# Optimization experiments

Hardware: AMD Instinct MI355X
Metric: run time of the kernel (lower is better)

Reference implementation:

```python
import jax, jax.numpy as jnp
import numpy as np

B, LQ, LA, D, H = 8, 2048, 2048, 300, 150

def setup_inputs() -> dict:
    key = jax.random.key(0)
    ks = jax.random.split(key, 6)
    return {
        "Q": jax.random.normal(ks[0], (B, LQ, D), dtype=jnp.float32),
        "A": jax.random.normal(ks[1], (B, LA, D), dtype=jnp.float32),
        "Wi": jax.random.normal(ks[2], (D, H), dtype=jnp.float32) * (1.0 / np.sqrt(D)),
        "Wu": jax.random.normal(ks[3], (D, H), dtype=jnp.float32) * (1.0 / np.sqrt(D)),
        "Wg": jax.random.normal(ks[4], (H, H), dtype=jnp.float32) * (1.0 / np.sqrt(H)),
        "Wt": jax.random.normal(ks[5], (2 * H, H), dtype=jnp.float32) * (1.0 / np.sqrt(2 * H)),
        "bi": jnp.zeros((H,), dtype=jnp.float32),
        "bu": jnp.zeros((H,), dtype=jnp.float32),
        "bg": jnp.zeros((H,), dtype=jnp.float32),
        "bt": jnp.zeros((H,), dtype=jnp.float32),
    }

def reference(Q, A, Wi, Wu, Wg, Wt, bi, bu, bg, bt):
    # sigmoid/tanh gated projections (shared weights for Q and A)
    def gate(X):
        return jax.nn.sigmoid(X @ Wi + bi) * jnp.tanh(X @ Wu + bu)
    Qh = gate(Q)  # [B, LQ, H]
    Ah = gate(A)  # [B, LA, H]
    # attention scores G[b,q,a] = <(Qh Wg + bg)[b,q], Ah[b,a]>
    G = jnp.einsum('bqh,bah->bqa', Qh @ Wg + bg, Ah)
    G = jax.nn.softmax(G, axis=1)  # softmax over Q positions
    # H[b,a] = sum_q G[b,q,a] * Qh[b,q]
    Hm = jnp.einsum('bqa,bqh->bah', G, Qh)  # [B, LA, H]
    # 'nn' comparison: relu(concat([Ah, Hm]) @ Wt + bt)
    T = jax.nn.relu(jnp.concatenate([Ah, Hm], axis=-1) @ Wt + bt)
    return T
```

## Files before the change

### kernel.cpp

```cpp
#include <hip/hip_runtime.h>
#include <math.h>

#define BB 8
#define LQ 2048
#define DD 300
#define HHH 150
#define NROWS (BB * LQ)

#define KP 168
#define QTS 72
#define WCE 27136
#define SLAB_B 45056
#define SLAB_E 22528
#define QHT_OFF_E 11008

typedef __bf16 bf16x8 __attribute__((ext_vector_type(8)));
typedef __bf16 bf16x4 __attribute__((ext_vector_type(4)));
typedef float f32x16 __attribute__((ext_vector_type(16)));

__device__ __forceinline__ void gl_lds16(const void* g, void* l) {
    __builtin_amdgcn_global_load_lds(
        (const __attribute__((address_space(1))) void*)g,
        (__attribute__((address_space(3))) void*)l,
        16, 0, 0);
}
__device__ __forceinline__ void stage_flat(const void* g, void* l, int bytes,
                                           int w, int lane) {
    for (int ofs = w * 1024; ofs < bytes; ofs += 4096)
        gl_lds16((const char*)g + ofs + lane * 16, (char*)l + ofs);
}
__device__ __forceinline__ void stage_flat8(const void* g, void* l, int bytes,
                                            int w, int lane) {
    for (int ofs = w * 1024; ofs < bytes; ofs += 8192)
        gl_lds16((const char*)g + ofs + lane * 16, (char*)l + ofs);
}
__device__ __forceinline__ f32x16 z16() {
    f32x16 v;
#pragma unroll
    for (int i = 0; i < 16; i++) v[i] = 0.f;
    return v;
}
__device__ __forceinline__ bf16x8 cvt8(float4 u, float4 v) {
    return (bf16x8){(__bf16)u.x, (__bf16)u.y, (__bf16)u.z, (__bf16)u.w,
                    (__bf16)v.x, (__bf16)v.y, (__bf16)v.z, (__bf16)v.w};
}

__global__ __launch_bounds__(256) void convert_weights(
    const float* __restrict__ Wi, const float* __restrict__ Wu,
    const float* __restrict__ Wg, const float* __restrict__ Wt,
    __bf16* __restrict__ WiC, __bf16* __restrict__ WuC,
    __bf16* __restrict__ WgT, __bf16* __restrict__ Wt12)
{
    const int z = blockIdx.y;
    const int i = blockIdx.x * 256 + threadIdx.x;
    if (z < 2) {
        if (i >= 2 * WCE) return;
        int c = i / WCE, rem = i - c * WCE;
        float v = 0.f;
        if (rem < 160 * KP) {
            int h = rem / KP, kc = rem - h * KP;
            int d = c * 160 + kc;
            if (kc < 160 && d < DD && h < HHH) v = (z ? Wu : Wi)[(size_t)d * HHH + h];
        }
        (z ? WuC : WiC)[i] = (__bf16)v;
    } else if (z == 2) {
        if (i >= WCE) return;
        float v = 0.f;
        if (i < 160 * KP) {
            int h = i / KP, kc = i - h * KP;
            if (kc < HHH && h < HHH) v = Wg[(size_t)kc * HHH + h];
        }
        WgT[i] = (__bf16)v;
    } else {
        if (i >= 2 * 160 * KP) return;
        int c = i / (160 * KP), rem = i - c * (160 * KP);
        int h = rem / KP, kc = rem - h * KP;
        float v = (kc < HHH && h < HHH) ? Wt[(size_t)(c * HHH + kc) * HHH + h] : 0.f;
        Wt12[i] = (__bf16)v;
    }
}

__global__ __launch_bounds__(512, 2) void gatep(
    const float* __restrict__ Q, const float* __restrict__ A,
    const __bf16* __restrict__ WiC, const __bf16* __restrict__ WuC,
    const __bf16* __restrict__ WgT,
    const float* __restrict__ bi, const float* __restrict__ bu,
    const float* __restrict__ bg,
    __bf16* __restrict__ AhB, __bf16* __restrict__ Slab)
{
    __shared__ __align__(16) __bf16 WB[2][WCE];
    __shared__ __align__(16) __bf16 QhA[128 * KP];
    const int tid = threadIdx.x;
    const int w = tid >> 6, lane = tid & 63;
    const int m32 = lane & 31, half = lane >> 5;
    const int wm = w & 3, wn = w >> 2;
    const int tof = wn ? 3 : 0, tn = wn ? 2 : 3;
    const int z = blockIdx.y;
    const int r0 = blockIdx.x * 128;
    const float* X = z ? A : Q;

    stage_flat8(WiC, WB[0], 54272, w, lane);

    const float* xrow = X + (size_t)(r0 + wm * 32 + m32) * DD + half * 8;
    bf16x8 af0[10], af1[10];
#pragma unroll
    for (int ks = 0; ks < 10; ks++) {
        float4 u = *(const float4*)(xrow + ks * 16);
        float4 v = *(const float4*)(xrow + ks * 16 + 4);
        af0[ks] = cvt8(u, v);
    }

    f32x16 ai[3], au[3];
#pragma unroll
    for (int t = 0; t < 3; t++) { ai[t] = z16(); au[t] = z16(); }

    __syncthreads();
    stage_flat8(WuC, WB[1], 54272, w, lane);

#pragma unroll
    for (int ks = 0; ks < 8; ks++) {
        float4 u = *(const float4*)(xrow + 160 + ks * 16);
        float4 v = *(const float4*)(xrow + 160 + ks * 16 + 4);
        af1[ks] = cvt8(u, v);
    }
    {
        float4 u = *(const float4*)(xrow + 288);
        float4 v = (half == 0) ? *(const float4*)(xrow + 292) : (float4){0.f, 0.f, 0.f, 0.f};
        af1[8] = cvt8(u, v);
        af1[9] = (bf16x8){(__bf16)0.f, (__bf16)0.f, (__bf16)0.f, (__bf16)0.f,
                          (__bf16)0.f, (__bf16)0.f, (__bf16)0.f, (__bf16)0.f};
    }

    for (int ks = 0; ks < 10; ks++)
#pragma unroll
        for (int ti = 0; ti < 3; ti++)
            if (ti < tn)
                ai[ti] = __builtin_amdgcn_mfma_f32_32x32x16_bf16(
                    af0[ks], *(const bf16x8*)(WB[0] + ((tof + ti) * 32 + m32) * KP + ks * 16 + half * 8),
                    ai[ti], 0, 0, 0);
    __syncthreads();
    stage_flat8(WiC + WCE, WB[0], 54272, w, lane);
    for (int ks = 0; ks < 10; ks++)
#pragma unroll
        for (int ti = 0; ti < 3; ti++)
            if (ti < tn)
                au[ti] = __builtin_amdgcn_mfma_f32_32x32x16_bf16(
                    af0[ks], *(const bf16x8*)(WB[1] + ((tof + ti) * 32 + m32) * KP + ks * 16 + half * 8),
                    au[ti], 0, 0, 0);
    __syncthreads();
    stage_flat8(WuC + WCE, WB[1], 54272, w, lane);
    for (int ks = 0; ks < 10; ks++)
#pragma unroll
        for (int ti = 0; ti < 3; ti++)
            if (ti < tn)
                ai[ti] = __builtin_amdgcn_mfma_f32_32x32x16_bf16(
                    af1[ks], *(const bf16x8*)(WB[0] + ((tof + ti) * 32 + m32) * KP + ks * 16 + half * 8),
                    ai[ti], 0, 0, 0);
    __syncthreads();
    if (z == 0) stage_flat8(WgT, WB[0], 54272, w, lane);
    for (int ks = 0; ks < 10; ks++)
#pragma unroll
        for (int ti = 0; ti < 3; ti++)
            if (ti < tn)
                au[ti] = __builtin_amdgcn_mfma_f32_32x32x16_bf16(
                    af1[ks], *(const bf16x8*)(WB[1] + ((tof + ti) * 32 + m32) * KP + ks * 16 + half * 8),
                    au[ti], 0, 0, 0);

#pragma unroll
    for (int ti = 0; ti < 3; ti++) {
        if (ti >= tn) continue;
        int h = (tof + ti) * 32 + m32;
        int hc = h < HHH ? h : 0;
        float bih = bi[hc], buh = bu[hc];
#pragma unroll
        for (int r = 0; r < 16; r++) {
            float v = 0.f;
            if (h < HHH) {
                float xi = ai[ti][r] + bih, xu = au[ti][r] + buh;
                float s = 1.f / (1.f + __expf(-xi));
                float tt = 1.f - 2.f / (1.f + __expf(2.f * xu));
                v = s * tt;
            }
            ai[ti][r] = v;
        }
    }

    if (z) {
#pragma unroll
        for (int ti = 0; ti < 3; ti++) {
            if (ti >= tn) continue;
            int h = (tof + ti) * 32 + m32;
#pragma unroll
            for (int r = 0; r < 16; r++) {
                int rowp = (r & 3) + 8 * (r >> 2) + 4 * half;
                AhB[(size_t)(r0 + wm * 32 + rowp) * KP + h] = (__bf16)ai[ti][r];
            }
        }
        return;
    }

#pragma unroll
    for (int ti = 0; ti < 3; ti++) {
        if (ti >= tn) continue;
        int h = (tof + ti) * 32 + m32;
#pragma unroll
        for (int r = 0; r < 16; r++) {
            int rowp = (r & 3) + 8 * (r >> 2) + 4 * half;
            QhA[(wm * 32 + rowp) * KP + h] = (__bf16)ai[ti][r];
        }
    }
    __syncthreads();

    bf16x8 afq[10];
#pragma unroll
    for (int ks = 0; ks < 10; ks++)
        afq[ks] = *(const bf16x8*)(QhA + (wm * 32 + m32) * KP + ks * 16 + half * 8);

    f32x16 qg[3];
#pragma unroll
    for (int t = 0; t < 3; t++) qg[t] = z16();
    for (int ks = 0; ks < 10; ks++)
#pragma unroll
        for (int ti = 0; ti < 3; ti++)
            if (ti < tn)
                qg[ti] = __builtin_amdgcn_mfma_f32_32x32x16_bf16(
                    afq[ks], *(const bf16x8*)(WB[0] + ((tof + ti) * 32 + m32) * KP + ks * 16 + half * 8),
                    qg[ti], 0, 0, 0);

    const int b = r0 >> 11, qt0 = (r0 & 2047) >> 6;
#pragma unroll
    for (int ti = 0; ti < 3; ti++) {
        if (ti >= tn) continue;
        int h = (tof + ti) * 32 + m32;
        int hc = h < HHH ? h : 0;
        float bgh = bg[hc];
#pragma unroll
        for (int r = 0; r < 16; r++) {
            int rowp = (r & 3) + 8 * (r >> 2) + 4 * half;
            int q = (r0 & 2047) + wm * 32 + rowp;
            float v = (h < HHH) ? (qg[ti][r] + bgh) : 0.f;
            Slab[(size_t)(b * 32 + (q >> 6)) * SLAB_E + (q & 63) * KP + h] = (__bf16)v;
        }
    }

    {
        const int jl = tid & 63, tile = (tid >> 6) & 1, hgrp = tid >> 7;
        for (int hseg = hgrp; hseg < 20; hseg += 4) {
            bf16x8 vv = *(const bf16x8*)(QhA + (tile * 64 + jl) * KP + hseg * 8);
            __bf16* dst = Slab + (size_t)(b * 32 + qt0 + tile) * SLAB_E + QHT_OFF_E + jl;
#pragma unroll
            for (int e = 0; e < 8; e++)
                dst[(hseg * 8 + e) * QTS] = vv[e];
        }
    }
}

__global__ __launch_bounds__(512, 2) void attn_mfma(
    const __bf16* __restrict__ Slab, const __bf16* __restrict__ AhB,
    __bf16* __restrict__ O, float* __restrict__ L)
{
    __shared__ __align__(16) __bf16 Buf[2][SLAB_E];
    __shared__ __align__(16) __bf16 PS[128 * QTS];
    const int tid = threadIdx.x;
    const int w = tid >> 6, lane = tid & 63;
    const int m32 = lane & 31, half = lane >> 5;
    const int wa = w & 3, wx = w >> 2;
    const int b = blockIdx.y, qh = blockIdx.z;
    const int a0 = blockIdx.x * 128;

    const char* slabBase = (const char*)Slab + (size_t)(b * 32 + qh * 16) * SLAB_B;
    stage_flat8(slabBase, Buf[0], SLAB_B, w, lane);

    const __bf16* arow = AhB + (size_t)(b * LQ + a0 + wa * 32 + m32) * KP + half * 8;
    bf16x8 af[10];
#pragma unroll
    for (int ks = 0; ks < 10; ks++)
        af[ks] = *(const bf16x8*)(arow + ks * 16);

    float lsum[16];
#pragma unroll
    for (int r = 0; r < 16; r++) lsum[r] = 0.f;
    f32x16 acc[5];
#pragma unroll
    for (int t = 0; t < 5; t++) acc[t] = z16();
    __syncthreads();

    for (int qt = 0; qt < 16; qt++) {
        const int cur = qt & 1;
        if (qt < 15)
            stage_flat8(slabBase + (size_t)(qt + 1) * SLAB_B, Buf[cur ^ 1], SLAB_B, w, lane);
        const __bf16* Bq = Buf[cur];
        const __bf16* Bv = Buf[cur] + QHT_OFF_E;

        f32x16 s = z16();
        for (int ks = 0; ks < 10; ks++)
            s = __builtin_amdgcn_mfma_f32_32x32x16_bf16(
                af[ks], *(const bf16x8*)(Bq + (wx * 32 + m32) * KP + ks * 16 + half * 8),
                s, 0, 0, 0);

#pragma unroll
        for (int r = 0; r < 16; r++) {
            int rowp = (r & 3) + 8 * (r >> 2) + 4 * half;
            float p = __expf(s[r]);
            lsum[r] += p;
            PS[(wa * 32 + rowp) * QTS + wx * 32 + m32] = (__bf16)p;
        }

#pragma unroll
        for (int kkL = 0; kkL < 2; kkL++) {
            bf16x8 pf = *(const bf16x8*)(PS + (wa * 32 + m32) * QTS + (wx * 2 + kkL) * 16 + half * 8);
#pragma unroll
            for (int t = 0; t < 5; t++)
                acc[t] = __builtin_amdgcn_mfma_f32_32x32x16_bf16(
                    pf, *(const bf16x8*)(Bv + (t * 32 + m32) * QTS + (wx * 2 + kkL) * 16 + half * 8),
                    acc[t], 0, 0, 0);
        }
        __syncthreads();
    }

#pragma unroll
    for (int r = 0; r < 16; r++) {
        float s = lsum[r];
#pragma unroll
        for (int m = 1; m < 32; m <<= 1) s += __shfl_xor(s, m, 64);
        lsum[r] = s;
    }
    const int part = qh * 2 + wx;
    __bf16* Ob = O + ((size_t)part * NROWS + b * LQ + a0 + wa * 32) * 160;
#pragma unroll
    for (int t = 0; t < 5; t++) {
        int h = t * 32 + m32;
#pragma unroll
        for (int r = 0; r < 16; r++) {
            int rowp = (r & 3) + 8 * (r >> 2) + 4 * half;
            Ob[(size_t)rowp * 160 + h] = (__bf16)acc[t][r];
        }
    }
    if (m32 == 0) {
        float* Lb = L + (size_t)part * NROWS + b * LQ + a0 + wa * 32;
#pragma unroll
        for (int r = 0; r < 16; r++) {
            int rowp = (r & 3) + 8 * (r >> 2) + 4 * half;
            Lb[rowp] = lsum[r];
        }
    }
}

__global__ __launch_bounds__(256, 1) void final_mfma(
    const __bf16* __restrict__ AhB, const __bf16* __restrict__ O,
    const float* __restrict__ L, const __bf16* __restrict__ Wt12,
    const float* __restrict__ bt, float* __restrict__ Out)
{
    __shared__ __align__(16) __bf16 AS[64 * KP];
    __shared__ __align__(16) __bf16 HS[64 * KP];
    __shared__ __align__(16) __bf16 WtS[2 * 160 * KP];
    const int tid = threadIdx.x;
    const int w = tid >> 6, lane = tid & 63;
    const int m32 = lane & 31, half = lane >> 5;
    const int r0 = blockIdx.x * 64;

    stage_flat(AhB + (size_t)r0 * KP, AS, 21504, w, lane);
    stage_flat(Wt12, WtS, 107520, w, lane);

    {
        int rhat = tid >> 2, qq = tid & 3;
        int grow = r0 + rhat;
        float inv = 1.f / (L[grow] + L[NROWS + grow] + L[2 * NROWS + grow] + L[3 * NROWS + grow]);
#pragma unroll
        for (int k = 0; k < 5; k++) {
            float sum[8];
#pragma unroll
            for (int j = 0; j < 8; j++) sum[j] = 0.f;
#pragma unroll
            for (int p = 0; p < 4; p++) {
                bf16x8 x = *(const bf16x8*)(O + ((size_t)p * NROWS + grow) * 160 + qq * 40 + k * 8);
#pragma unroll
                for (int j = 0; j < 8; j++) sum[j] += (float)x[j];
            }
            bf16x8 hv;
#pragma unroll
            for (int j = 0; j < 8; j++) hv[j] = (__bf16)(sum[j] * inv);
            *(bf16x8*)(HS + rhat * KP + qq * 40 + k * 8) = hv;
        }
    }
    __syncthreads();

    const int m = w & 1, th = w >> 1;
    const int tbase = th ? 3 : 0, tn = th ? 2 : 3;
    f32x16 acc[3];
#pragma unroll
    for (int i = 0; i < 3; i++) acc[i] = z16();

    for (int ch = 0; ch < 2; ch++) {
        const __bf16* src = ch ? HS : AS;
        for (int ks = 0; ks < 10; ks++) {
            bf16x8 af = *(const bf16x8*)(src + (m * 32 + m32) * KP + ks * 16 + half * 8);
#pragma unroll
            for (int ti = 0; ti < 3; ti++) {
                if (ti < tn) {
                    int t = tbase + ti;
                    acc[ti] = __builtin_amdgcn_mfma_f32_32x32x16_bf16(
                        af, *(const bf16x8*)(WtS + (ch * 160 + t * 32 + m32) * KP + ks * 16 + half * 8),
                        acc[ti], 0, 0, 0);
                }
            }
        }
    }

#pragma unroll
    for (int ti = 0; ti < 3; ti++) {
        if (ti < tn) {
            int t = tbase + ti;
            int h = t * 32 + m32;
            if (h < HHH) {
                float bth = bt[h];
#pragma unroll
                for (int r = 0; r < 16; r++) {
                    int rowp = (r & 3) + 8 * (r >> 2) + 4 * half;
                    float v = acc[ti][r] + bth;
                    Out[(size_t)(r0 + m * 32 + rowp) * HHH + h] = v > 0.f ? v : 0.f;
                }
            }
        }
    }
}

extern "C" void kernel_launch(void* const* d_in, const int* in_sizes, int n_in,
                              void* d_out, int out_size, void* d_ws, size_t ws_size,
                              hipStream_t stream)
{
    const float* Q  = (const float*)d_in[0];
    const float* A  = (const float*)d_in[1];
    const float* Wi = (const float*)d_in[2];
    const float* Wu = (const float*)d_in[3];
    const float* Wg = (const float*)d_in[4];
    const float* Wt = (const float*)d_in[5];
    const float* bi = (const float*)d_in[6];
    const float* bu = (const float*)d_in[7];
    const float* bg = (const float*)d_in[8];
    const float* bt = (const float*)d_in[9];
    float* out = (float*)d_out;

    char* ws = (char*)d_ws;
    __bf16* Slab = (__bf16*)(ws);
    __bf16* AhB  = (__bf16*)(ws + 11534336);
    __bf16* Op   = (__bf16*)(ws + 17039360);
    float*  Lp   = (float*) (ws + 38010880);
    __bf16* WiC  = (__bf16*)(ws + 38273024);
    __bf16* WuC  = (__bf16*)(ws + 38381568);
    __bf16* WgT  = (__bf16*)(ws + 38490112);
    __bf16* Wt12 = (__bf16*)(ws + 38544384);

    convert_weights<<<dim3(212, 4), 256, 0, stream>>>(Wi, Wu, Wg, Wt,
                                                      WiC, WuC, WgT, Wt12);
    gatep<<<dim3(NROWS / 128, 2), 512, 0, stream>>>(Q, A, WiC, WuC, WgT,
                                                    bi, bu, bg, AhB, Slab);
    attn_mfma<<<dim3(16, BB, 2), 512, 0, stream>>>(Slab, AhB, Op, Lp);
    final_mfma<<<NROWS / 64, 256, 0, stream>>>(AhB, Op, Lp, Wt12, bt, out);
}
```

Baseline: 167.3 us.

## Retile attention kernel so each wave owns 32 A rows across full Q tile

The attention kernel now gives each of its 8 waves 32 distinct A rows (256 rows per block) and has each wave cover the whole 64-wide Q tile, instead of splitting the Q tile between two waves. The Q range per block halves to 8 tiles and the grid gains a fourth Q partition. This removes the duplicated A-row work across waves and halves the number of slab tiles each block streams, raising MFMA work per staged LDS tile. In exchange it adds a larger PS buffer in LDS, more accumulator registers per wave, and four partial outputs instead of four per row, so occupancy may change.

```diff
diff --git a/kernel.cpp b/kernel.cpp
--- a/kernel.cpp
+++ b/kernel.cpp
@@ -260,18 +260,17 @@
     __bf16* __restrict__ O, float* __restrict__ L)
 {
     __shared__ __align__(16) __bf16 Buf[2][SLAB_E];
-    __shared__ __align__(16) __bf16 PS[128 * QTS];
+    __shared__ __align__(16) __bf16 PS[256 * QTS];
     const int tid = threadIdx.x;
     const int w = tid >> 6, lane = tid & 63;
     const int m32 = lane & 31, half = lane >> 5;
-    const int wa = w & 3, wx = w >> 2;
-    const int b = blockIdx.y, qh = blockIdx.z;
-    const int a0 = blockIdx.x * 128;
-
-    const char* slabBase = (const char*)Slab + (size_t)(b * 32 + qh * 16) * SLAB_B;
+    const int b = blockIdx.y, qp = blockIdx.z;
+    const int a0 = blockIdx.x * 256;
+
+    const char* slabBase = (const char*)Slab + (size_t)(b * 32 + qp * 8) * SLAB_B;
     stage_flat8(slabBase, Buf[0], SLAB_B, w, lane);
 
-    const __bf16* arow = AhB + (size_t)(b * LQ + a0 + wa * 32 + m32) * KP + half * 8;
+    const __bf16* arow = AhB + (size_t)(b * LQ + a0 + w * 32 + m32) * KP + half * 8;
     bf16x8 af[10];
 #pragma unroll
     for (int ks = 0; ks < 10; ks++)
@@ -285,34 +284,38 @@
     for (int t = 0; t < 5; t++) acc[t] = z16();
     __syncthreads();
 
-    for (int qt = 0; qt < 16; qt++) {
+    for (int qt = 0; qt < 8; qt++) {
         const int cur = qt & 1;
-        if (qt < 15)
+        if (qt < 7)
             stage_flat8(slabBase + (size_t)(qt + 1) * SLAB_B, Buf[cur ^ 1], SLAB_B, w, lane);
         const __bf16* Bq = Buf[cur];
         const __bf16* Bv = Buf[cur] + QHT_OFF_E;
 
-        f32x16 s = z16();
-        for (int ks = 0; ks < 10; ks++)
-            s = __builtin_amdgcn_mfma_f32_32x32x16_bf16(
-                af[ks], *(const bf16x8*)(Bq + (wx * 32 + m32) * KP + ks * 16 + half * 8),
-                s, 0, 0, 0);
+        f32x16 s0 = z16(), s1 = z16();
+        for (int ks = 0; ks < 10; ks++) {
+            bf16x8 b0 = *(const bf16x8*)(Bq + m32 * KP + ks * 16 + half * 8);
+            bf16x8 b1 = *(const bf16x8*)(Bq + (32 + m32) * KP + ks * 16 + half * 8);
+            s0 = __builtin_amdgcn_mfma_f32_32x32x16_bf16(af[ks], b0, s0, 0, 0, 0);
+            s1 = __builtin_amdgcn_mfma_f32_32x32x16_bf16(af[ks], b1, s1, 0, 0, 0);
+        }
 
 #pragma unroll
         for (int r = 0; r < 16; r++) {
             int rowp = (r & 3) + 8 * (r >> 2) + 4 * half;
-            float p = __expf(s[r]);
-            lsum[r] += p;
-            PS[(wa * 32 + rowp) * QTS + wx * 32 + m32] = (__bf16)p;
-        }
-
-#pragma unroll
-        for (int kkL = 0; kkL < 2; kkL++) {
-            bf16x8 pf = *(const bf16x8*)(PS + (wa * 32 + m32) * QTS + (wx * 2 + kkL) * 16 + half * 8);
+            float p0 = __expf(s0[r]);
+            float p1 = __expf(s1[r]);
+            PS[(w * 32 + rowp) * QTS + m32] = (__bf16)p0;
+            PS[(w * 32 + rowp) * QTS + 32 + m32] = (__bf16)p1;
+            lsum[r] += p0 + p1;
+        }
+
+#pragma unroll
+        for (int kk = 0; kk < 4; kk++) {
+            bf16x8 pf = *(const bf16x8*)(PS + (w * 32 + m32) * QTS + kk * 16 + half * 8);
 #pragma unroll
             for (int t = 0; t < 5; t++)
                 acc[t] = __builtin_amdgcn_mfma_f32_32x32x16_bf16(
-                    pf, *(const bf16x8*)(Bv + (t * 32 + m32) * QTS + (wx * 2 + kkL) * 16 + half * 8),
+                    pf, *(const bf16x8*)(Bv + (t * 32 + m32) * QTS + kk * 16 + half * 8),
                     acc[t], 0, 0, 0);
         }
         __syncthreads();
@@ -325,8 +328,7 @@
         for (int m = 1; m < 32; m <<= 1) s += __shfl_xor(s, m, 64);
         lsum[r] = s;
     }
-    const int part = qh * 2 + wx;
-    __bf16* Ob = O + ((size_t)part * NROWS + b * LQ + a0 + wa * 32) * 160;
+    __bf16* Ob = O + ((size_t)qp * NROWS + b * LQ + a0 + w * 32) * 160;
 #pragma unroll
     for (int t = 0; t < 5; t++) {
         int h = t * 32 + m32;
@@ -337,7 +339,7 @@
         }
     }
     if (m32 == 0) {
-        float* Lb = L + (size_t)part * NROWS + b * LQ + a0 + wa * 32;
+        float* Lb = L + (size_t)qp * NROWS + b * LQ + a0 + w * 32;
 #pragma unroll
         for (int r = 0; r < 16; r++) {
             int rowp = (r & 3) + 8 * (r >> 2) + 4 * half;
@@ -455,6 +457,6 @@
                                                       WiC, WuC, WgT, Wt12);
     gatep<<<dim3(NROWS / 128, 2), 512, 0, stream>>>(Q, A, WiC, WuC, WgT,
                                                     bi, bu, bg, AhB, Slab);
-    attn_mfma<<<dim3(16, BB, 2), 512, 0, stream>>>(Slab, AhB, Op, Lp);
+    attn_mfma<<<dim3(8, BB, 4), 512, 0, stream>>>(Slab, AhB, Op, Lp);
     final_mfma<<<NROWS / 64, 256, 0, stream>>>(AhB, Op, Lp, Wt12, bt, out);
 }
```

New measurement: 161.4 us. 1.04x faster.
